# Optimization experiments

Hardware: AMD Instinct MI355X
Metric: run time of the kernel (lower is better)

Reference implementation:

```python
import math
import jax, jax.numpy as jnp
import numpy as np

B, T, C, HS = 4, 4096, 1024, 64  # batch, seq, n_embd, head_size=n_embd//n_head

def setup_inputs() -> dict:
    key = jax.random.key(0)
    k0, k1, k2, k3 = jax.random.split(key, 4)
    x = jax.random.normal(k0, (B, T, C), dtype=jnp.float32)
    Wq = jax.random.normal(k1, (C, HS), dtype=jnp.float32) * 0.02
    Wk = jax.random.normal(k2, (C, HS), dtype=jnp.float32) * 0.02
    Wv = jax.random.normal(k3, (C, HS), dtype=jnp.float32) * 0.02
    return {"x": x, "Wq": Wq, "Wk": Wk, "Wv": Wv}

def reference(x, Wq, Wk, Wv):
    b, t, c = x.shape
    q = x @ Wq                                   # [B,T,hs]
    k = x @ Wk                                   # [B,T,hs]
    v = x @ Wv                                   # [B,T,hs]
    wei = jnp.einsum('btd,bsd->bts', q, k)       # [B,T,T] raw scores
    row_sums = wei.sum(axis=-1)                  # [B,T]
    k_sel = math.ceil(t / 2)                     # static: t known at trace time
    _, idx = jax.lax.top_k(row_sums, k_sel)      # [B,k_sel]
    idx = jnp.sort(idx, axis=1)
    # gather selected score rows: [B,k_sel,T]
    half_wei = jnp.take_along_axis(wei, idx[:, :, None], axis=1)
    # causal mask rows gathered from tril: tril[idx[b,i], j] == (j <= idx[b,i])
    half_mask = jnp.arange(t)[None, None, :] <= idx[:, :, None]  # [B,k_sel,T] bool
    half_wei = half_wei * (c ** -0.5)            # NOTE: scaled by n_embd, as in source
    half_wei = jnp.where(half_mask, half_wei, -jnp.inf)
    att = jax.nn.softmax(half_wei, axis=-1)      # [B,k_sel,T]
    out = att @ v                                # [B,k_sel,hs]
    return out
```

## Files before the change

### kernel.cpp

```cpp
#include <hip/hip_runtime.h>
#include <math.h>

#define BB 4
#define TT 4096
#define CC 1024
#define HS 64
#define KSEL 2048
#define NEG (-1e30f)
#define NSPL 16
#define SWLOG 8
#define SW 256

typedef float f32x4 __attribute__((ext_vector_type(4)));
typedef short short8 __attribute__((ext_vector_type(8)));

__device__ __forceinline__ unsigned short f2bf(float f) {
  union { float f; unsigned int u; } c;
  c.f = f;
  const unsigned int u = c.u;
  return (unsigned short)((u + 0x7FFFu + ((u >> 16) & 1u)) >> 16);
}

__device__ __forceinline__ unsigned cvtpk(float lo, float hi) {
  unsigned r;
  asm("v_cvt_pk_bf16_f32 %0, %1, %2" : "=v"(r) : "v"(lo), "v"(hi));
  return r;
}

__global__ __launch_bounds__(256) void conv_w(const float* __restrict__ Wq,
                                              const float* __restrict__ Wk,
                                              const float* __restrict__ Wv,
                                              unsigned short* __restrict__ wbf) {
  const int gid = blockIdx.x * 256 + threadIdx.x;
  const int kt = gid / 768;
  const int rem = gid - kt * 768;
  const int nt = rem >> 6, lane = rem & 63;
  const int col = nt * 16 + (lane & 15);
  const float* W = (col < 64) ? Wq : ((col < 128) ? Wk : Wv);
  const int cl = col & 63;
  const int k0 = kt * 32 + (lane >> 4) * 8;
  unsigned short tmp[8];
#pragma unroll
  for (int i = 0; i < 8; i++) tmp[i] = f2bf(W[(size_t)(k0 + i) * HS + cl]);
  uint4 o;
  o.x = tmp[0] | ((unsigned)tmp[1] << 16);
  o.y = tmp[2] | ((unsigned)tmp[3] << 16);
  o.z = tmp[4] | ((unsigned)tmp[5] << 16);
  o.w = tmp[6] | ((unsigned)tmp[7] << 16);
  *(uint4*)(wbf + (size_t)gid * 8) = o;
}

#define PR 32
__global__ __launch_bounds__(256) void fusedproj(
    const float* __restrict__ x, const unsigned short* __restrict__ wbf,
    float* __restrict__ xsum, unsigned short* __restrict__ qbf,
    unsigned short* __restrict__ kbf, unsigned short* __restrict__ vtbf) {
  __shared__ unsigned short Xs[PR][256];
  __shared__ float xsred[4][256];
  const int rb = blockIdx.x;
  const size_t r0 = (size_t)rb * PR;
  const int tid = threadIdx.x;
  const int wid = tid >> 6, lane = tid & 63;
  const int lhi = lane >> 4, llo = lane & 15;
  const int mt = wid >> 1, nh = wid & 1;
  const int cl = tid & 63, rg = tid >> 6;
  const int bidx = rb >> 7;

  f32x4 acc[6];
#pragma unroll
  for (int n = 0; n < 6; n++) acc[n] = (f32x4){0.f, 0.f, 0.f, 0.f};

  float4 pf[8];
#pragma unroll
  for (int rr = 0; rr < 8; rr++)
    pf[rr] = *(const float4*)(x + (r0 + rg * 8 + rr) * CC + cl * 4);

  for (int ch = 0; ch < 4; ch++) {
    float ps0 = 0.f, ps1 = 0.f, ps2 = 0.f, ps3 = 0.f;
#pragma unroll
    for (int rr = 0; rr < 8; rr++) {
      const int row = rg * 8 + rr;
      float4 v = pf[rr];
      ps0 += v.x; ps1 += v.y; ps2 += v.z; ps3 += v.w;
      *(uint2*)((char*)&Xs[0][0] + row * 512 +
                ((((cl >> 1) ^ (row & 7))) << 4) + ((cl & 1) << 3)) =
          make_uint2(cvtpk(v.x, v.y), cvtpk(v.z, v.w));
    }
    xsred[rg][cl * 4 + 0] = ps0;
    xsred[rg][cl * 4 + 1] = ps1;
    xsred[rg][cl * 4 + 2] = ps2;
    xsred[rg][cl * 4 + 3] = ps3;
    __syncthreads();
    if (ch < 3) {
#pragma unroll
      for (int rr = 0; rr < 8; rr++)
        pf[rr] = *(const float4*)(x + (r0 + rg * 8 + rr) * CC +
                                  (ch + 1) * 256 + cl * 4);
    }
    atomicAdd(&xsum[bidx * CC + ch * 256 + tid],
              xsred[0][tid] + xsred[1][tid] + xsred[2][tid] + xsred[3][tid]);
    const int row = mt * 16 + llo;
#pragma unroll
    for (int ktl = 0; ktl < 8; ktl++) {
      short8 af = *(const short8*)((const char*)&Xs[0][0] + row * 512 +
                                   ((((ktl << 2) + lhi) ^ (row & 7)) << 4));
      const unsigned short* bp =
          wbf + (((size_t)(ch * 8 + ktl) * 12 + nh * 6) * 64 + lane) * 8;
#pragma unroll
      for (int n = 0; n < 6; n++) {
        short8 bf = *(const short8*)(bp + n * 64 * 8);
        acc[n] = __builtin_amdgcn_mfma_f32_16x16x32_bf16(af, bf, acc[n], 0, 0, 0);
      }
    }
    __syncthreads();
  }
  const int rbg = (int)r0 + mt * 16 + lhi * 4;
#pragma unroll
  for (int n = 0; n < 6; n++) {
    const int col = (nh * 6 + n) * 16 + llo;
    const int mat = col >> 6, cl2 = col & 63;
    if (mat == 0) {
#pragma unroll
      for (int r = 0; r < 4; r++)
        qbf[(size_t)(rbg + r) * HS + cl2] = f2bf(acc[n][r] * 0.03125f);
    } else if (mat == 1) {
#pragma unroll
      for (int r = 0; r < 4; r++)
        kbf[(size_t)(rbg + r) * HS + cl2] = f2bf(acc[n][r]);
    } else {
      const int bb = rbg >> 12, tloc = rbg & (TT - 1);
      *(uint2*)(vtbf + ((size_t)bb * HS + cl2) * TT + tloc) =
          make_uint2(cvtpk(acc[n][0], acc[n][1]), cvtpk(acc[n][2], acc[n][3]));
    }
  }
}

__global__ __launch_bounds__(512) void rowsums_x(
    const float* __restrict__ x, const float* __restrict__ Wq,
    const float* __restrict__ Wk, const float* __restrict__ xsum,
    float* __restrict__ rs) {
  __shared__ float xsl[CC];
  __shared__ float kred[8][HS];
  __shared__ float ksl[HS];
  __shared__ float wl[CC];
  const int g = blockIdx.x;
  const int tid = threadIdx.x;
  const int b = g >> 6;
  *(float2*)(xsl + tid * 2) = *(const float2*)(xsum + b * CC + tid * 2);
  __syncthreads();
  {
    const int g8 = tid >> 6, d = tid & 63;
    const float* wkp = Wk + (size_t)(g8 * 128) * HS + d;
    float s = 0.f;
    for (int c = 0; c < 128; c++) s += xsl[g8 * 128 + c] * wkp[(size_t)c * HS];
    kred[g8][d] = s;
  }
  __syncthreads();
  if (tid < 64) {
    float s = 0.f;
#pragma unroll
    for (int g8 = 0; g8 < 8; g8++) s += kred[g8][tid];
    ksl[tid] = s;
  }
  __syncthreads();
#pragma unroll
  for (int p = 0; p < 2; p++) {
    const int c = tid * 2 + p;
    const float* wqp = Wq + (size_t)c * HS;
    float s = 0.f;
#pragma unroll
    for (int d4 = 0; d4 < 16; d4++) {
      float4 a = *(const float4*)(wqp + d4 * 4);
      float4 kk = *(const float4*)(ksl + d4 * 4);
      s += a.x * kk.x + a.y * kk.y + a.z * kk.z + a.w * kk.w;
    }
    wl[c] = s;
  }
  __syncthreads();
  const size_t row = (size_t)g * 64 + (tid >> 3);
  const int qu = tid & 7;
  const float* xr = x + row * CC + qu * 128;
  const float* wr = wl + qu * 128;
  float s = 0.f;
  for (int e = 0; e < 32; e++) {
    float4 v = *(const float4*)(xr + e * 4);
    float4 w4 = *(const float4*)(wr + e * 4);
    s += v.x * w4.x + v.y * w4.y + v.z * w4.z + v.w * w4.w;
  }
  s += __shfl_xor(s, 1);
  s += __shfl_xor(s, 2);
  s += __shfl_xor(s, 4);
  if (qu == 0) rs[row] = s;
}

__global__ __launch_bounds__(256) void rankk(const float* __restrict__ rs,
                                             int* __restrict__ flag) {
  __shared__ float rl[TT];
  const int g = blockIdx.x;
  const int b = g >> 7, chunk = g & 127;
  const int tid = threadIdx.x;
  const float* rsb = rs + (size_t)b * TT;
  for (int e = tid; e < TT / 4; e += 256)
    *(float4*)(rl + e * 4) = *(const float4*)(rsb + e * 4);
  __syncthreads();
  const int cand = tid >> 3, qu = tid & 7;
  const int t = chunk * 32 + cand;
  const float my = rl[t];
  int cnt = 0;
  for (int e = 0; e < 128; e++) {
    const int s = qu * 512 + e * 4;
    float4 v = *(const float4*)(rl + s);
    cnt += (v.x > my) || (v.x == my && (s + 0) < t);
    cnt += (v.y > my) || (v.y == my && (s + 1) < t);
    cnt += (v.z > my) || (v.z == my && (s + 2) < t);
    cnt += (v.w > my) || (v.w == my && (s + 3) < t);
  }
  cnt += __shfl_xor(cnt, 1);
  cnt += __shfl_xor(cnt, 2);
  cnt += __shfl_xor(cnt, 4);
  if (qu == 0) flag[(size_t)b * TT + t] = (cnt < KSEL) ? 1 : 0;
}

__global__ __launch_bounds__(256) void compact(const int* __restrict__ flag,
                                               int* __restrict__ idx) {
  __shared__ int sums[256];
  const int b = blockIdx.x;
  const int tid = threadIdx.x;
  const int* fb = flag + (size_t)b * TT;
  const int base = tid * 16;
  int f[16];
  int cnt = 0;
#pragma unroll
  for (int e = 0; e < 16; e++) { f[e] = fb[base + e]; cnt += f[e]; }
  sums[tid] = cnt;
  __syncthreads();
  for (int d = 1; d < 256; d <<= 1) {
    int v = (tid >= d) ? sums[tid - d] : 0;
    __syncthreads();
    sums[tid] += v;
    __syncthreads();
  }
  int pos = sums[tid] - cnt;
#pragma unroll
  for (int e = 0; e < 16; e++)
    if (f[e]) idx[(size_t)b * KSEL + (pos++)] = base + e;
}

struct KF { short8 a0, a1, b0, b1; };
struct VF { short8 v0, v1, v2, v3; };

__global__ __launch_bounds__(256) void attn_mfma(
    const unsigned short* __restrict__ qbf,
    const unsigned short* __restrict__ kbf,
    const unsigned short* __restrict__ vtbf, const int* __restrict__ idx,
    float* __restrict__ pl, float* __restrict__ pacc) {
  __shared__ unsigned short P_lds[4][32][40];
  const int rb = blockIdx.x;
  const int zz = blockIdx.y;
  const int b = blockIdx.z;
  const int tid = threadIdx.x;
  const int wid = tid >> 6, lane = tid & 63;
  const int s = zz * 4 + wid;
  const size_t rbase = (size_t)b * KSEL + rb * 32;
  const int tmaxblk = idx[rbase + 31];
  const int jlo = s << SWLOG;
  if (jlo > tmaxblk) return;

  const int lhi = lane >> 4, llo = lane & 15;
  const int trow0 = idx[rbase + llo];
  const int trow1 = idx[rbase + 16 + llo];
  short8 qf[2][2];
  {
    const unsigned short* qp0 = qbf + ((size_t)b * TT + trow0) * HS + lhi * 8;
    const unsigned short* qp1 = qbf + ((size_t)b * TT + trow1) * HS + lhi * 8;
    qf[0][0] = *(const short8*)(qp0);
    qf[0][1] = *(const short8*)(qp0 + 32);
    qf[1][0] = *(const short8*)(qp1);
    qf[1][1] = *(const short8*)(qp1 + 32);
  }
  f32x4 o[2][4];
#pragma unroll
  for (int mtt = 0; mtt < 2; mtt++)
#pragma unroll
    for (int n = 0; n < 4; n++) o[mtt][n] = (f32x4){0.f, 0.f, 0.f, 0.f};
  float lsum[2] = {0.f, 0.f};

  const unsigned short* kb = kbf + (size_t)b * TT * HS;
  const unsigned short* vb = vtbf + (size_t)b * HS * TT;
  const int jend = min(tmaxblk + 1, jlo + SW);

  auto loadK = [&](int j0) {
    KF K;
    const unsigned short* kp = kb + (size_t)(j0 + llo) * HS + lhi * 8;
    K.a0 = *(const short8*)(kp);
    K.a1 = *(const short8*)(kp + 32);
    K.b0 = *(const short8*)(kp + 16 * HS);
    K.b1 = *(const short8*)(kp + 16 * HS + 32);
    return K;
  };
  auto loadV = [&](int j0) {
    VF V;
    const unsigned short* vp = vb + (size_t)llo * TT + j0 + lhi * 8;
    V.v0 = *(const short8*)(vp);
    V.v1 = *(const short8*)(vp + 16 * TT);
    V.v2 = *(const short8*)(vp + 32 * TT);
    V.v3 = *(const short8*)(vp + 48 * TT);
    return V;
  };

  auto body = [&](int j0, const KF& K, const VF& V) {
    f32x4 sc[2][2];
#pragma unroll
    for (int mtt = 0; mtt < 2; mtt++) {
      f32x4 a = (f32x4){0.f, 0.f, 0.f, 0.f};
      a = __builtin_amdgcn_mfma_f32_16x16x32_bf16(K.a0, qf[mtt][0], a, 0, 0, 0);
      a = __builtin_amdgcn_mfma_f32_16x16x32_bf16(K.a1, qf[mtt][1], a, 0, 0, 0);
      sc[mtt][0] = a;
      f32x4 c = (f32x4){0.f, 0.f, 0.f, 0.f};
      c = __builtin_amdgcn_mfma_f32_16x16x32_bf16(K.b0, qf[mtt][0], c, 0, 0, 0);
      c = __builtin_amdgcn_mfma_f32_16x16x32_bf16(K.b1, qf[mtt][1], c, 0, 0, 0);
      sc[mtt][1] = c;
    }
#pragma unroll
    for (int mtt = 0; mtt < 2; mtt++) {
      const int tr = (mtt == 0) ? trow0 : trow1;
      float p[8];
#pragma unroll
      for (int kt = 0; kt < 2; kt++)
#pragma unroll
        for (int r = 0; r < 4; r++) {
          const int kk = j0 + kt * 16 + lhi * 4 + r;
          const float e = __expf(sc[mtt][kt][r]);
          p[kt * 4 + r] = (kk <= tr) ? e : 0.f;
        }
      lsum[mtt] += ((p[0] + p[1]) + (p[2] + p[3])) +
                   ((p[4] + p[5]) + (p[6] + p[7]));
      *(uint2*)&P_lds[wid][mtt * 16 + llo][lhi * 4] =
          make_uint2(cvtpk(p[0], p[1]), cvtpk(p[2], p[3]));
      *(uint2*)&P_lds[wid][mtt * 16 + llo][16 + lhi * 4] =
          make_uint2(cvtpk(p[4], p[5]), cvtpk(p[6], p[7]));
    }
    short8 pa0 = *(const short8*)&P_lds[wid][llo][lhi * 8];
    short8 pa1 = *(const short8*)&P_lds[wid][16 + llo][lhi * 8];
    o[0][0] = __builtin_amdgcn_mfma_f32_16x16x32_bf16(pa0, V.v0, o[0][0], 0, 0, 0);
    o[1][0] = __builtin_amdgcn_mfma_f32_16x16x32_bf16(pa1, V.v0, o[1][0], 0, 0, 0);
    o[0][1] = __builtin_amdgcn_mfma_f32_16x16x32_bf16(pa0, V.v1, o[0][1], 0, 0, 0);
    o[1][1] = __builtin_amdgcn_mfma_f32_16x16x32_bf16(pa1, V.v1, o[1][1], 0, 0, 0);
    o[0][2] = __builtin_amdgcn_mfma_f32_16x16x32_bf16(pa0, V.v2, o[0][2], 0, 0, 0);
    o[1][2] = __builtin_amdgcn_mfma_f32_16x16x32_bf16(pa1, V.v2, o[1][2], 0, 0, 0);
    o[0][3] = __builtin_amdgcn_mfma_f32_16x16x32_bf16(pa0, V.v3, o[0][3], 0, 0, 0);
    o[1][3] = __builtin_amdgcn_mfma_f32_16x16x32_bf16(pa1, V.v3, o[1][3], 0, 0, 0);
  };

  int j0 = jlo;
  KF ka = loadK(j0), kb2;
  VF va = loadV(j0), vb2;
  for (;;) {
    if (j0 + 32 < jend) { kb2 = loadK(j0 + 32); vb2 = loadV(j0 + 32); }
    body(j0, ka, va);
    j0 += 32;
    if (j0 >= jend) break;
    if (j0 + 32 < jend) { ka = loadK(j0 + 32); va = loadV(j0 + 32); }
    body(j0, kb2, vb2);
    j0 += 32;
    if (j0 >= jend) break;
  }

  lsum[0] += __shfl_xor(lsum[0], 16);
  lsum[0] += __shfl_xor(lsum[0], 32);
  lsum[1] += __shfl_xor(lsum[1], 16);
  lsum[1] += __shfl_xor(lsum[1], 32);
  if (lane < 16) {
    pl[(rbase + llo) * NSPL + s] = lsum[0];
    pl[(rbase + 16 + llo) * NSPL + s] = lsum[1];
  }
#pragma unroll
  for (int mtt = 0; mtt < 2; mtt++)
#pragma unroll
    for (int r = 0; r < 4; r++) {
      const size_t rowi = rbase + mtt * 16 + lhi * 4 + r;
#pragma unroll
      for (int n = 0; n < 4; n++)
        pacc[(rowi * NSPL + s) * HS + n * 16 + llo] = o[mtt][n][r];
    }
}

__global__ __launch_bounds__(256) void attn_combine(
    const float* __restrict__ pl, const float* __restrict__ pacc,
    const int* __restrict__ idx, float* __restrict__ out) {
  const int b = blockIdx.x;
  const int i0 = blockIdx.y * 32;
  const int tid = threadIdx.x;
  const int r = tid >> 3, dg = tid & 7;
  const size_t rowi = (size_t)b * KSEL + i0 + r;
  const int t_r = idx[rowi];
  const int ns = (t_r >> SWLOG) + 1;
  float L = 0.f;
  float o[8] = {0.f, 0.f, 0.f, 0.f, 0.f, 0.f, 0.f, 0.f};
  for (int s = 0; s < ns; s++) {
    L += pl[rowi * NSPL + s];
    const float* pa = pacc + (rowi * NSPL + s) * HS + dg * 8;
    float4 a0 = *(const float4*)(pa);
    float4 a1 = *(const float4*)(pa + 4);
    o[0] += a0.x; o[1] += a0.y; o[2] += a0.z; o[3] += a0.w;
    o[4] += a1.x; o[5] += a1.y; o[6] += a1.z; o[7] += a1.w;
  }
  const float invl = 1.0f / L;
  float* op = out + rowi * HS + dg * 8;
  *(float4*)(op) = make_float4(o[0] * invl, o[1] * invl, o[2] * invl, o[3] * invl);
  *(float4*)(op + 4) = make_float4(o[4] * invl, o[5] * invl, o[6] * invl, o[7] * invl);
}

extern "C" void kernel_launch(void* const* d_in, const int* in_sizes, int n_in,
                              void* d_out, int out_size, void* d_ws,
                              size_t ws_size, hipStream_t stream) {
  const float* x = (const float*)d_in[0];
  const float* Wq = (const float*)d_in[1];
  const float* Wk = (const float*)d_in[2];
  const float* Wv = (const float*)d_in[3];
  float* out = (float*)d_out;

  float* wsf = (float*)d_ws;
  float* pacc = wsf;
  float* xsum = wsf;
  float* rs = xsum + 4096;
  int* flag = (int*)(rs + 16384);
  unsigned short* wbf = (unsigned short*)(flag + 16384);
  unsigned short* qbf = (unsigned short*)(pacc + 8388608);
  unsigned short* kbf = qbf + 1048576;
  unsigned short* vtbf = kbf + 1048576;
  int* idxp = (int*)(vtbf + 1048576);
  float* pl = (float*)(idxp + 8192);

  hipMemsetAsync(xsum, 0, BB * CC * sizeof(float), stream);
  conv_w<<<96, 256, 0, stream>>>(Wq, Wk, Wv, wbf);
  fusedproj<<<512, 256, 0, stream>>>(x, wbf, xsum, qbf, kbf, vtbf);
  rowsums_x<<<256, 512, 0, stream>>>(x, Wq, Wk, xsum, rs);
  rankk<<<512, 256, 0, stream>>>(rs, flag);
  compact<<<BB, 256, 0, stream>>>(flag, idxp);
  attn_mfma<<<dim3(64, 4, BB), 256, 0, stream>>>(qbf, kbf, vtbf, idxp, pl, pacc);
  attn_combine<<<dim3(BB, 64), 256, 0, stream>>>(pl, pacc, idxp, out);
}
```

Before: 128.6 us.

## Double-buffer projection LDS, halve row tile, fold memset, warp-scan compact

The projection kernel now processes 16 rows per block across 1024 blocks. It double-buffers the bf16 X tile and the column-sum partials, so the next chunk's conversion overlaps the MFMAs and one barrier per chunk goes away. The xsum zeroing moves into conv_w, which removes a separate memset launch. The compact kernel replaces its LDS Hillis-Steele scan with a wavefront shuffle scan and vectorised flag loads. Together these aim to cut launch, barrier and latency overhead, at the cost of twice as many atomicAdds on xsum and more LDS per block.

Result: slower. 136.0 us (+5.7%).

```diff
diff --git a/kernel.cpp b/kernel.cpp
--- a/kernel.cpp
+++ b/kernel.cpp
@@ -6,7 +6,6 @@
 #define CC 1024
 #define HS 64
 #define KSEL 2048
-#define NEG (-1e30f)
 #define NSPL 16
 #define SWLOG 8
 #define SW 256
@@ -30,8 +29,11 @@
 __global__ __launch_bounds__(256) void conv_w(const float* __restrict__ Wq,
                                               const float* __restrict__ Wk,
                                               const float* __restrict__ Wv,
-                                              unsigned short* __restrict__ wbf) {
+                                              unsigned short* __restrict__ wbf,
+                                              float* __restrict__ xsum) {
   const int gid = blockIdx.x * 256 + threadIdx.x;
+  if (gid < 1024)
+    ((float4*)xsum)[gid] = make_float4(0.f, 0.f, 0.f, 0.f);
   const int kt = gid / 768;
   const int rem = gid - kt * 768;
   const int nt = rem >> 6, lane = rem & 63;
@@ -50,74 +52,93 @@
   *(uint4*)(wbf + (size_t)gid * 8) = o;
 }
 
-#define PR 32
+#define PR 16
 __global__ __launch_bounds__(256) void fusedproj(
     const float* __restrict__ x, const unsigned short* __restrict__ wbf,
     float* __restrict__ xsum, unsigned short* __restrict__ qbf,
     unsigned short* __restrict__ kbf, unsigned short* __restrict__ vtbf) {
-  __shared__ unsigned short Xs[PR][256];
-  __shared__ float xsred[4][256];
+  __shared__ unsigned short Xs[2][PR][256];
+  __shared__ float xsred[2][4][256];
   const int rb = blockIdx.x;
   const size_t r0 = (size_t)rb * PR;
   const int tid = threadIdx.x;
   const int wid = tid >> 6, lane = tid & 63;
   const int lhi = lane >> 4, llo = lane & 15;
-  const int mt = wid >> 1, nh = wid & 1;
   const int cl = tid & 63, rg = tid >> 6;
-  const int bidx = rb >> 7;
-
-  f32x4 acc[6];
-#pragma unroll
-  for (int n = 0; n < 6; n++) acc[n] = (f32x4){0.f, 0.f, 0.f, 0.f};
-
-  float4 pf[8];
-#pragma unroll
-  for (int rr = 0; rr < 8; rr++)
-    pf[rr] = *(const float4*)(x + (r0 + rg * 8 + rr) * CC + cl * 4);
-
-  for (int ch = 0; ch < 4; ch++) {
+  const int bidx = rb >> 8;
+
+  f32x4 acc[3];
+#pragma unroll
+  for (int n = 0; n < 3; n++) acc[n] = (f32x4){0.f, 0.f, 0.f, 0.f};
+
+  float4 pf[4];
+#pragma unroll
+  for (int rr = 0; rr < 4; rr++)
+    pf[rr] = *(const float4*)(x + (r0 + rg * 4 + rr) * CC + cl * 4);
+
+  {
     float ps0 = 0.f, ps1 = 0.f, ps2 = 0.f, ps3 = 0.f;
 #pragma unroll
-    for (int rr = 0; rr < 8; rr++) {
-      const int row = rg * 8 + rr;
+    for (int rr = 0; rr < 4; rr++) {
+      const int row = rg * 4 + rr;
       float4 v = pf[rr];
       ps0 += v.x; ps1 += v.y; ps2 += v.z; ps3 += v.w;
-      *(uint2*)((char*)&Xs[0][0] + row * 512 +
+      *(uint2*)((char*)&Xs[0][0][0] + row * 512 +
                 ((((cl >> 1) ^ (row & 7))) << 4) + ((cl & 1) << 3)) =
           make_uint2(cvtpk(v.x, v.y), cvtpk(v.z, v.w));
     }
-    xsred[rg][cl * 4 + 0] = ps0;
-    xsred[rg][cl * 4 + 1] = ps1;
-    xsred[rg][cl * 4 + 2] = ps2;
-    xsred[rg][cl * 4 + 3] = ps3;
-    __syncthreads();
+    xsred[0][rg][cl * 4 + 0] = ps0;
+    xsred[0][rg][cl * 4 + 1] = ps1;
+    xsred[0][rg][cl * 4 + 2] = ps2;
+    xsred[0][rg][cl * 4 + 3] = ps3;
+  }
+  __syncthreads();
+
+  for (int ch = 0; ch < 4; ch++) {
+    const int cur = ch & 1;
     if (ch < 3) {
 #pragma unroll
-      for (int rr = 0; rr < 8; rr++)
-        pf[rr] = *(const float4*)(x + (r0 + rg * 8 + rr) * CC +
+      for (int rr = 0; rr < 4; rr++)
+        pf[rr] = *(const float4*)(x + (r0 + rg * 4 + rr) * CC +
                                   (ch + 1) * 256 + cl * 4);
     }
     atomicAdd(&xsum[bidx * CC + ch * 256 + tid],
-              xsred[0][tid] + xsred[1][tid] + xsred[2][tid] + xsred[3][tid]);
-    const int row = mt * 16 + llo;
+              xsred[cur][0][tid] + xsred[cur][1][tid] + xsred[cur][2][tid] +
+                  xsred[cur][3][tid]);
 #pragma unroll
     for (int ktl = 0; ktl < 8; ktl++) {
-      short8 af = *(const short8*)((const char*)&Xs[0][0] + row * 512 +
-                                   ((((ktl << 2) + lhi) ^ (row & 7)) << 4));
+      short8 af = *(const short8*)((const char*)&Xs[cur][0][0] + llo * 512 +
+                                   ((((ktl << 2) + lhi) ^ (llo & 7)) << 4));
       const unsigned short* bp =
-          wbf + (((size_t)(ch * 8 + ktl) * 12 + nh * 6) * 64 + lane) * 8;
-#pragma unroll
-      for (int n = 0; n < 6; n++) {
+          wbf + (((size_t)(ch * 8 + ktl) * 12 + wid * 3) * 64 + lane) * 8;
+#pragma unroll
+      for (int n = 0; n < 3; n++) {
         short8 bf = *(const short8*)(bp + n * 64 * 8);
         acc[n] = __builtin_amdgcn_mfma_f32_16x16x32_bf16(af, bf, acc[n], 0, 0, 0);
       }
     }
-    __syncthreads();
-  }
-  const int rbg = (int)r0 + mt * 16 + lhi * 4;
-#pragma unroll
-  for (int n = 0; n < 6; n++) {
-    const int col = (nh * 6 + n) * 16 + llo;
+    if (ch < 3) {
+      float ps0 = 0.f, ps1 = 0.f, ps2 = 0.f, ps3 = 0.f;
+#pragma unroll
+      for (int rr = 0; rr < 4; rr++) {
+        const int row = rg * 4 + rr;
+        float4 v = pf[rr];
+        ps0 += v.x; ps1 += v.y; ps2 += v.z; ps3 += v.w;
+        *(uint2*)((char*)&Xs[cur ^ 1][0][0] + row * 512 +
+                  ((((cl >> 1) ^ (row & 7))) << 4) + ((cl & 1) << 3)) =
+            make_uint2(cvtpk(v.x, v.y), cvtpk(v.z, v.w));
+      }
+      xsred[cur ^ 1][rg][cl * 4 + 0] = ps0;
+      xsred[cur ^ 1][rg][cl * 4 + 1] = ps1;
+      xsred[cur ^ 1][rg][cl * 4 + 2] = ps2;
+      xsred[cur ^ 1][rg][cl * 4 + 3] = ps3;
+      __syncthreads();
+    }
+  }
+  const int rbg = (int)r0 + lhi * 4;
+#pragma unroll
+  for (int n = 0; n < 3; n++) {
+    const int col = (wid * 3 + n) * 16 + llo;
     const int mat = col >> 6, cl2 = col & 63;
     if (mat == 0) {
 #pragma unroll
@@ -223,24 +244,37 @@
 
 __global__ __launch_bounds__(256) void compact(const int* __restrict__ flag,
                                                int* __restrict__ idx) {
-  __shared__ int sums[256];
+  __shared__ int wsum[4];
+  __shared__ int woff[4];
   const int b = blockIdx.x;
   const int tid = threadIdx.x;
+  const int wid = tid >> 6, lane = tid & 63;
   const int* fb = flag + (size_t)b * TT;
   const int base = tid * 16;
   int f[16];
   int cnt = 0;
 #pragma unroll
-  for (int e = 0; e < 16; e++) { f[e] = fb[base + e]; cnt += f[e]; }
-  sums[tid] = cnt;
-  __syncthreads();
-  for (int d = 1; d < 256; d <<= 1) {
-    int v = (tid >= d) ? sums[tid - d] : 0;
-    __syncthreads();
-    sums[tid] += v;
-    __syncthreads();
-  }
-  int pos = sums[tid] - cnt;
+  for (int e4 = 0; e4 < 4; e4++) {
+    int4 v = *(const int4*)(fb + base + e4 * 4);
+    f[e4 * 4 + 0] = v.x; f[e4 * 4 + 1] = v.y;
+    f[e4 * 4 + 2] = v.z; f[e4 * 4 + 3] = v.w;
+    cnt += v.x + v.y + v.z + v.w;
+  }
+  int sc = cnt;
+#pragma unroll
+  for (int d = 1; d < 64; d <<= 1) {
+    int v = __shfl_up(sc, d);
+    if (lane >= d) sc += v;
+  }
+  if (lane == 63) wsum[wid] = sc;
+  __syncthreads();
+  if (tid == 0) {
+    int a = 0;
+#pragma unroll
+    for (int w = 0; w < 4; w++) { woff[w] = a; a += wsum[w]; }
+  }
+  __syncthreads();
+  int pos = woff[wid] + sc - cnt;
 #pragma unroll
   for (int e = 0; e < 16; e++)
     if (f[e]) idx[(size_t)b * KSEL + (pos++)] = base + e;
@@ -432,9 +466,8 @@
   int* idxp = (int*)(vtbf + 1048576);
   float* pl = (float*)(idxp + 8192);
 
-  hipMemsetAsync(xsum, 0, BB * CC * sizeof(float), stream);
-  conv_w<<<96, 256, 0, stream>>>(Wq, Wk, Wv, wbf);
-  fusedproj<<<512, 256, 0, stream>>>(x, wbf, xsum, qbf, kbf, vtbf);
+  conv_w<<<96, 256, 0, stream>>>(Wq, Wk, Wv, wbf, xsum);
+  fusedproj<<<1024, 256, 0, stream>>>(x, wbf, xsum, qbf, kbf, vtbf);
   rowsums_x<<<256, 512, 0, stream>>>(x, Wq, Wk, xsum, rs);
   rankk<<<512, 256, 0, stream>>>(rs, flag);
   compact<<<BB, 256, 0, stream>>>(flag, idxp);
```
